# Optimization experiments

Measured on AMD Instinct MI355X. Metric: run time of the kernel, lower is better.

## Reference

```python
import jax, jax.numpy as jnp
import numpy as np

B, T, N, C = 4, 12, 200, 64
ATT = 128      # hard-coded attention_dim in GCN_OPERATION
H = 64         # AdjGen LSTM hidden size
DA = 64        # AdjGen adjacency projection dim
OUT_F = 128    # num_of_out_features
PRED = 12      # predict_length
NFILT = 3      # len(filters) per STSGCM
DATA_LEN = T - 4  # after 2 STSGCL layers


def setup_inputs() -> dict:
    key = jax.random.key(0)
    ks = jax.random.split(key, 16)
    s = 0.05
    f32 = jnp.float32
    return {
        "x": jax.random.normal(ks[0], (B, T, N, C), f32),
        "cur_epi": 5,
        "his_hn": jax.random.normal(ks[1], (B, H), f32),
        "his_cn": jax.random.normal(ks[2], (B, H), f32),
        "Wqkv": jax.random.normal(ks[3], (C, 3 * ATT), f32) * s,
        "bqkv": jnp.zeros((3 * ATT,), f32),
        "Wlin": jax.random.normal(ks[4], (ATT, C), f32) * s,
        "blin": jnp.zeros((C,), f32),
        "Wa": jax.random.normal(ks[5], (C, DA), f32) * s,
        "Wb": jax.random.normal(ks[6], (C, DA), f32) * s,
        "Wx_lstm": jax.random.normal(ks[7], (C, 4 * H), f32) * s,
        "Wh_lstm": jax.random.normal(ks[8], (H, 4 * H), f32) * s,
        "b_lstm": jnp.zeros((4 * H,), f32),
        "temb0": jax.random.normal(ks[9], (1, T, 1, C), f32) * 0.01,
        "temb1": jax.random.normal(ks[10], (1, T - 2, 1, C), f32) * 0.01,
        "semb": jax.random.normal(ks[11], (1, 1, N, C), f32) * 0.01,
        "Wo": jax.random.normal(ks[12], (DATA_LEN * C, OUT_F), f32) * s,
        "bo": jnp.zeros((OUT_F,), f32),
    }


def _forward(x, his_hn, his_cn, Wqkv, bqkv, Wlin, blin, Wa, Wb,
             Wx_lstm, Wh_lstm, b_lstm, temb0, temb1, semb, Wo, bo):
    dt = x.dtype
    att_scale = jnp.sqrt(jnp.asarray(float(ATT), dt))
    adj_scale = jnp.sqrt(jnp.asarray(float(DA), dt))

    def adjgen(xw):
        # xw: (B, nw, M, C). Stand-in for AdjGen (source unavailable):
        # content-dependent learned adjacency over M=3N nodes + one LSTM step.
        node = xw.mean(axis=(0, 1))                                  # (M, C)
        logits = (node @ Wa) @ (node @ Wb).T / adj_scale             # (M, M)
        adj = jax.nn.sigmoid(logits)
        pooled = xw.mean(axis=(1, 2))                                # (B, C)
        gates = pooled @ Wx_lstm + his_hn @ Wh_lstm + b_lstm
        i, f, g, o = jnp.split(gates, 4, axis=-1)
        c_n = jax.nn.sigmoid(f) * his_cn + jax.nn.sigmoid(i) * jnp.tanh(g)
        h_n = jax.nn.sigmoid(o) * jnp.tanh(c_n)
        return adj, logits, h_n, c_n

    def gcn_op(xw, adj):
        # QK^T softmax attention rescaled by adj, renormalized, then AV.
        Bn, nw, M, Cc = xw.shape
        xf = xw.reshape(Bn * nw, M, Cc)
        qkv = xf @ Wqkv + bqkv
        q, k, v = jnp.split(qkv, 3, axis=-1)                          # (BW, M, ATT)
        scores = jnp.einsum('bmd,bnd->bmn', q, k) / att_scale         # (BW, M, M)
        aw = jax.nn.softmax(scores, axis=-1) * adj
        ssum = aw.sum(-1, keepdims=True)
        mask = (ssum > 0).astype(dt)
        w = aw / (ssum + 1e-8) * mask
        out = jnp.einsum('bmn,bnd->bmd', w, jax.nn.relu(v)) @ Wlin + blin
        return out.reshape(Bn, nw, M, -1)

    def stsgcm(xw, Nn):
        cands = []
        cur = xw
        hn = cn = None
        for _ in range(NFILT):
            adj, _logits, hn, cn = adjgen(cur)
            cur = gcn_op(cur, adj)
            Bn, nw, M, F = cur.shape
            # keep only the middle-window copy of the N vertices: [2N:3N]
            cands.append(cur.reshape(Bn * nw, M, F)[:, 2 * Nn:3 * Nn, :])
        out = jnp.max(jnp.stack(cands, axis=0), axis=0)               # (B*nw, N, F)
        return out, hn, cn

    def stsgcl(xw, temb):
        Bn, Tt, Nn, Cc = xw.shape
        xw = xw + temb + semb                                         # position embedding
        nw = Tt - 2
        idx = jnp.arange(nw)[:, None] + jnp.arange(3)[None, :]        # (nw, 3)
        t_all = xw[:, idx].reshape(Bn, nw, 3 * Nn, Cc)
        out, hn, cn = stsgcm(t_all, Nn)
        return out.reshape(Bn, nw, Nn, -1), hn, cn

    h, hn, cn = stsgcl(x, temb0)
    h, hn, cn = stsgcl(h, temb1)
    # OUTPUT layer: (B, T', N, F) -> (B, N, T'*F) -> ReLU(Linear) -> tile PRED times on dim 1
    Bn, Tt, Nn, F = h.shape
    d = h.transpose(0, 2, 1, 3).reshape(Bn, Nn, Tt * F)
    o1 = jax.nn.relu(d @ Wo + bo)                                     # (B, N, OUT_F)
    return jnp.tile(o1, (1, PRED, 1))                                 # (B, PRED*N, OUT_F)


def reference(x, cur_epi, his_hn, his_cn, Wqkv, bqkv, Wlin, blin, Wa, Wb,
              Wx_lstm, Wh_lstm, b_lstm, temb0, temb1, semb, Wo, bo):
    del cur_epi  # annealing schedule of the (unavailable) AdjGen; unused here
    return _forward(x, his_hn, his_cn, Wqkv, bqkv, Wlin, blin, Wa, Wb,
                    Wx_lstm, Wh_lstm, b_lstm, temb0, temb1, semb, Wo, bo)
```

## Files before the change

### kernel.cpp

```cpp
#include <hip/hip_runtime.h>
#include <hip/hip_bf16.h>
#include <math.h>

constexpr int Bc   = 4;
constexpr int Nc   = 200;
constexpr int Cc   = 64;
constexpr int Mc   = 600;
constexpr int ATTc = 128;
constexpr int OUTFc = 128;
constexpr int PREDc = 12;
constexpr int MAXBW = 40;
constexpr int MPAD  = 640;

typedef short short4v __attribute__((ext_vector_type(4)));
typedef short short8 __attribute__((ext_vector_type(8)));
typedef float f32x4  __attribute__((ext_vector_type(4)));

static __device__ __forceinline__ void bsplit(float v, short& h, short& l) {
    __hip_bfloat16 hb = __float2bfloat16(v);
    float hf = __bfloat162float(hb);
    __hip_bfloat16 lb = __float2bfloat16(v - hf);
    h = *(short*)&hb; l = *(short*)&lb;
}

__global__ __launch_bounds__(256)
void embed_window_k(const float* __restrict__ src, const float* __restrict__ temb,
                    const float* __restrict__ semb, float* __restrict__ dst,
                    int Tin, int nw, long total)
{
    long idx = (long)blockIdx.x * 256 + threadIdx.x;
    if (idx >= total) return;
    int c = (int)(idx & 63);
    long r = idx >> 6;
    int n = (int)(r % Nc); r /= Nc;
    int j = (int)(r % 3);  r /= 3;
    int w = (int)(r % nw);
    int b = (int)(r / nw);
    int t = w + j;
    dst[idx] = src[(((long)b * Tin + t) * Nc + n) * Cc + c]
             + temb[t * Cc + c] + semb[n * Cc + c];
}

__global__ __launch_bounds__(256)
void mean_nab_k(const float* __restrict__ cur, const float* __restrict__ Wa,
                const float* __restrict__ Wb,
                ushort* __restrict__ NAH, ushort* __restrict__ NAL,
                ushort* __restrict__ NBH, ushort* __restrict__ NBL, int BW)
{
    __shared__ float Ns[64][17];
    __shared__ float Ws[64][132];
    const int m0 = blockIdx.x * 16;
    const int t = threadIdx.x;
    for (int e = t; e < 1024; e += 256) {
        int r = e >> 4, c4 = (e & 15) << 2;
        *(float4*)&Ws[r][c4]      = *(const float4*)&Wa[r * 64 + c4];
        *(float4*)&Ws[r][64 + c4] = *(const float4*)&Wb[r * 64 + c4];
    }
    {
        int row = t >> 4, c4 = (t & 15) << 2;
        int gm = m0 + row;
        float4 sv = make_float4(0.f, 0.f, 0.f, 0.f);
        if (gm < Mc) {
            for (int bw = 0; bw < BW; bw++) {
                const float4 v = *(const float4*)&cur[((long)bw * Mc + gm) * Cc + c4];
                sv.x += v.x; sv.y += v.y; sv.z += v.z; sv.w += v.w;
            }
        }
        const float inv = 1.f / BW;
        Ns[c4 + 0][row] = sv.x * inv; Ns[c4 + 1][row] = sv.y * inv;
        Ns[c4 + 2][row] = sv.z * inv; Ns[c4 + 3][row] = sv.w * inv;
    }
    __syncthreads();
    const int row = t >> 4, c8 = (t & 15) * 8;
    float acc[8] = {};
    for (int k = 0; k < 64; k++) {
        float a = Ns[k][row];
        float b[8];
        *(float4*)&b[0] = *(const float4*)&Ws[k][c8];
        *(float4*)&b[4] = *(const float4*)&Ws[k][c8 + 4];
#pragma unroll
        for (int j = 0; j < 8; j++) acc[j] += a * b[j];
    }
    int gm = m0 + row;
    if (gm < Mc) {
#pragma unroll
        for (int j = 0; j < 8; j++) {
            int col = c8 + j;
            short h, l;
            bsplit(acc[j], h, l);
            if (col < 64) { NAH[gm * 64 + col] = (ushort)h; NAL[gm * 64 + col] = (ushort)l; }
            else { NBH[gm * 64 + col - 64] = (ushort)h; NBL[gm * 64 + col - 64] = (ushort)l; }
        }
    }
}

__global__ __launch_bounds__(256)
void prep_k(const float* __restrict__ Wlin,
            ushort* __restrict__ WTH, ushort* __restrict__ WTL,
            const float* __restrict__ Wqkv,
            ushort* __restrict__ WQH, ushort* __restrict__ WQL)
{
    int i = blockIdx.x * 256 + threadIdx.x;
    if (i < 64 * 128) {
        int c = i >> 7, a = i & 127;
        short h, l;
        bsplit(Wlin[a * 64 + c], h, l);
        WTH[c * 128 + a] = (ushort)h;
        WTL[c * 128 + a] = (ushort)l;
    } else {
        int j = i - 64 * 128;
        if (j < 384 * 64) {
            int n = j >> 6, c = j & 63;
            short h, l;
            bsplit(Wqkv[c * 384 + n], h, l);
            WQH[n * 64 + c] = (ushort)h;
            WQL[n * 64 + c] = (ushort)l;
        }
    }
}

__global__ __launch_bounds__(256)
void qkv_adj_k(const float* __restrict__ CURp,
               const ushort* __restrict__ WQH, const ushort* __restrict__ WQL,
               const float* __restrict__ bias,
               ushort* __restrict__ QH, ushort* __restrict__ QL,
               ushort* __restrict__ KH, ushort* __restrict__ KL,
               ushort* __restrict__ VTH, ushort* __restrict__ VTL,
               const ushort* __restrict__ Ah, const ushort* __restrict__ Al,
               const ushort* __restrict__ Bh, const ushort* __restrict__ Bl,
               float* __restrict__ ADJ, int nqkv)
{
    __shared__ __align__(16) ushort SM[36864];
    const int t = threadIdx.x;
    const int lane = t & 63, w = t >> 6;
    const int lm = lane & 15, lq = lane >> 4;

    if ((int)blockIdx.x >= nqkv) {
        const int b2 = blockIdx.x - nqkv;
        const int m0 = (b2 / 5) * 128, n0 = (b2 % 5) * 128;
        ushort (*As)[128][40] = (ushort (*)[128][40])(SM);
        ushort (*Bs)[128][40] = (ushort (*)[128][40])(SM + 10240);
        const int wm = (w >> 1) * 64, wn = (w & 1) * 64;

        f32x4 acc[4][4];
#pragma unroll
        for (int i = 0; i < 4; i++)
#pragma unroll
            for (int j = 0; j < 4; j++)
#pragma unroll
                for (int r = 0; r < 4; r++) acc[i][j][r] = 0.f;

        for (int k0 = 0; k0 < 64; k0 += 32) {
            __syncthreads();
#pragma unroll
            for (int p = 0; p < 2; p++) {
                int e = t + p * 256;
                int row = e >> 2, ks = (e & 3) << 3;
                {
                    int gm = m0 + row;
                    short8 vh, vl;
#pragma unroll
                    for (int q = 0; q < 8; q++) { vh[q] = 0; vl[q] = 0; }
                    if (gm < Mc) {
                        vh = *(const short8*)(Ah + (long)gm * 64 + k0 + ks);
                        vl = *(const short8*)(Al + (long)gm * 64 + k0 + ks);
                    }
                    *(short8*)&As[0][row][ks] = vh;
                    *(short8*)&As[1][row][ks] = vl;
                }
                {
                    int gn = n0 + row;
                    short8 vh, vl;
#pragma unroll
                    for (int q = 0; q < 8; q++) { vh[q] = 0; vl[q] = 0; }
                    if (gn < Mc) {
                        vh = *(const short8*)(Bh + (long)gn * 64 + k0 + ks);
                        vl = *(const short8*)(Bl + (long)gn * 64 + k0 + ks);
                    }
                    *(short8*)&Bs[0][row][ks] = vh;
                    *(short8*)&Bs[1][row][ks] = vl;
                }
            }
            __syncthreads();

            short8 af[4][2], bf[4][2];
#pragma unroll
            for (int i = 0; i < 4; i++) {
                af[i][0] = *(const short8*)&As[0][wm + i * 16 + lm][lq * 8];
                af[i][1] = *(const short8*)&As[1][wm + i * 16 + lm][lq * 8];
            }
#pragma unroll
            for (int j = 0; j < 4; j++) {
                bf[j][0] = *(const short8*)&Bs[0][wn + j * 16 + lm][lq * 8];
                bf[j][1] = *(const short8*)&Bs[1][wn + j * 16 + lm][lq * 8];
            }
#pragma unroll
            for (int i = 0; i < 4; i++)
#pragma unroll
                for (int j = 0; j < 4; j++) {
                    acc[i][j] = __builtin_amdgcn_mfma_f32_16x16x32_bf16(af[i][0], bf[j][0], acc[i][j], 0, 0, 0);
                    acc[i][j] = __builtin_amdgcn_mfma_f32_16x16x32_bf16(af[i][0], bf[j][1], acc[i][j], 0, 0, 0);
                    acc[i][j] = __builtin_amdgcn_mfma_f32_16x16x32_bf16(af[i][1], bf[j][0], acc[i][j], 0, 0, 0);
                }
        }
#pragma unroll
        for (int i = 0; i < 4; i++) {
            int gmb = m0 + wm + i * 16 + lq * 4;
#pragma unroll
            for (int j = 0; j < 4; j++) {
                int gn = n0 + wn + j * 16 + lm;
                if (gn >= Mc) continue;
#pragma unroll
                for (int r = 0; r < 4; r++) {
                    int gm = gmb + r;
                    if (gm < Mc)
                        ADJ[(long)gm * Mc + gn] = 1.f / (1.f + __expf(-acc[i][j][r] * 0.125f));
                }
            }
        }
        return;
    }

    ushort* AsH = SM;
    ushort* AsL = SM + 9216;
    ushort* BsH = SM + 18432;
    ushort* BsL = SM + 27648;
    const int bid = blockIdx.x;
    const int xcd = bid & 7, slot = bid >> 3;
    const int z = (slot / 15) * 8 + xcd;
    const int r15 = slot % 15;
    const int which = r15 % 3;
    const int m0 = (r15 / 3) * 128;
    const int nb = which * 128;
    const float* A = CURp + (long)z * Mc * Cc;
    const int wm = (w >> 1) * 64, wn = (w & 1) * 64;

#pragma unroll
    for (int p = 0; p < 8; p++) {
        int e = t + p * 256;
        int row = e >> 4, k4 = (e & 15) * 4;
        int gm = m0 + row;
        float4 v = make_float4(0.f, 0.f, 0.f, 0.f);
        if (gm < Mc) v = *(const float4*)(A + (long)gm * 64 + k4);
        short4v h4, l4;
        short hs, ls;
        bsplit(v.x, hs, ls); h4[0] = hs; l4[0] = ls;
        bsplit(v.y, hs, ls); h4[1] = hs; l4[1] = ls;
        bsplit(v.z, hs, ls); h4[2] = hs; l4[2] = ls;
        bsplit(v.w, hs, ls); h4[3] = hs; l4[3] = ls;
        *(short4v*)(AsH + row * 72 + k4) = h4;
        *(short4v*)(AsL + row * 72 + k4) = l4;
    }
#pragma unroll
    for (int p = 0; p < 4; p++) {
        int e = t + p * 256;
        int row = e >> 3, seg = (e & 7) * 8;
        *(short8*)(BsH + row * 72 + seg) = *(const short8*)(WQH + (long)(nb + row) * 64 + seg);
        *(short8*)(BsL + row * 72 + seg) = *(const short8*)(WQL + (long)(nb + row) * 64 + seg);
    }
    __syncthreads();

    f32x4 acc[4][4];
#pragma unroll
    for (int i = 0; i < 4; i++)
#pragma unroll
        for (int j = 0; j < 4; j++)
#pragma unroll
            for (int r = 0; r < 4; r++) acc[i][j][r] = 0.f;

#pragma unroll
    for (int ks = 0; ks < 2; ks++) {
        short8 af[4][2], bf[4][2];
#pragma unroll
        for (int i = 0; i < 4; i++) {
            af[i][0] = *(const short8*)(AsH + (wm + i * 16 + lm) * 72 + ks * 32 + lq * 8);
            af[i][1] = *(const short8*)(AsL + (wm + i * 16 + lm) * 72 + ks * 32 + lq * 8);
        }
#pragma unroll
        for (int j = 0; j < 4; j++) {
            bf[j][0] = *(const short8*)(BsH + (wn + j * 16 + lm) * 72 + ks * 32 + lq * 8);
            bf[j][1] = *(const short8*)(BsL + (wn + j * 16 + lm) * 72 + ks * 32 + lq * 8);
        }
#pragma unroll
        for (int i = 0; i < 4; i++)
#pragma unroll
            for (int j = 0; j < 4; j++) {
                acc[i][j] = __builtin_amdgcn_mfma_f32_16x16x32_bf16(af[i][0], bf[j][0], acc[i][j], 0, 0, 0);
                acc[i][j] = __builtin_amdgcn_mfma_f32_16x16x32_bf16(af[i][0], bf[j][1], acc[i][j], 0, 0, 0);
                acc[i][j] = __builtin_amdgcn_mfma_f32_16x16x32_bf16(af[i][1], bf[j][0], acc[i][j], 0, 0, 0);
            }
    }
    __syncthreads();

    uint* CP = (uint*)SM;
#pragma unroll
    for (int i = 0; i < 4; i++)
#pragma unroll
        for (int j = 0; j < 4; j++) {
            int col = wn + j * 16 + lm;
            float b = bias[nb + col];
#pragma unroll
            for (int r = 0; r < 4; r++) {
                int row = wm + i * 16 + lq * 4 + r;
                float v = acc[i][j][r] + b;
                if (which == 2) v = fmaxf(v, 0.f);
                short hs, ls;
                bsplit(v, hs, ls);
                CP[row * 132 + col] = ((uint)(ushort)ls << 16) | (uint)(ushort)hs;
            }
        }
    __syncthreads();

    if (which == 2) {
        ushort* vh = VTH + (long)z * ATTc * MPAD;
        ushort* vl = VTL + (long)z * ATTc * MPAD;
#pragma unroll
        for (int p = 0; p < 8; p++) {
            int e = t + p * 256;
            int col = e >> 4, rg = (e & 15) * 8;
            if (m0 + rg < Mc) {
                short8 h8, l8;
#pragma unroll
                for (int q = 0; q < 8; q++) {
                    uint u = CP[(rg + q) * 132 + col];
                    h8[q] = (short)(u & 0xffff);
                    l8[q] = (short)(u >> 16);
                }
                *(short8*)(vh + (long)col * MPAD + m0 + rg) = h8;
                *(short8*)(vl + (long)col * MPAD + m0 + rg) = l8;
            }
        }
    } else {
        ushort* dh = (which == 0 ? QH : KH) + (long)z * Mc * ATTc;
        ushort* dl = (which == 0 ? QL : KL) + (long)z * Mc * ATTc;
#pragma unroll
        for (int p = 0; p < 8; p++) {
            int e = t + p * 256;
            int row = e >> 4, seg = (e & 15) * 8;
            int gm = m0 + row;
            if (gm < Mc) {
                short8 h8, l8;
#pragma unroll
                for (int q = 0; q < 8; q++) {
                    uint u = CP[row * 132 + seg + q];
                    h8[q] = (short)(u & 0xffff);
                    l8[q] = (short)(u >> 16);
                }
                *(short8*)(dh + (long)gm * ATTc + seg) = h8;
                *(short8*)(dl + (long)gm * ATTc + seg) = l8;
            }
        }
    }
}

#define ISSUE_K(Dh, Dl, kc_, g_)                                        \
  _Pragma("unroll")                                                     \
  for (int p = 0; p < 4; p++) {                                         \
    int key = (kc_) + srow0 + 32 * p;                                   \
    short8 vh, vl;                                                      \
    _Pragma("unroll")                                                   \
    for (int q2 = 0; q2 < 8; q2++) { vh[q2] = 0; vl[q2] = 0; }          \
    if (key < Mc) {                                                     \
      vh = *(const short8*)(Khz + (long)key * ATTc + (g_) * 64 + sks);  \
      vl = *(const short8*)(Klz + (long)key * ATTc + (g_) * 64 + sks);  \
    }                                                                   \
    Dh[p] = vh; Dl[p] = vl;                                             \
  }

#define ISSUE_V(Dh, Dl, kc_, g_)                                                   \
  _Pragma("unroll")                                                                \
  for (int p = 0; p < 4; p++) {                                                    \
    int att = srow0 + 32 * p;                                                      \
    Dh[p] = *(const short8*)(Vhz + (long)att * MPAD + (kc_) + (g_) * 64 + sks);    \
    Dl[p] = *(const short8*)(Vlz + (long)att * MPAD + (kc_) + (g_) * 64 + sks);    \
  }

#define WRITE_SB(Dh, Dl)                                                \
  _Pragma("unroll")                                                     \
  for (int p = 0; p < 4; p++) {                                         \
    *(short8*)&SB[0][srow0 + 32 * p][sks] = Dh[p];                      \
    *(short8*)&SB[1][srow0 + 32 * p][sks] = Dl[p];                      \
  }

#define MFMA_QK(base_)                                                   \
  _Pragma("unroll")                                                      \
  for (int kk = 0; kk < 2; kk++) {                                       \
    _Pragma("unroll")                                                    \
    for (int j = 0; j < 8; j++) {                                        \
      short8 bh = *(const short8*)&SB[0][j * 16 + lm][kk * 32 + lq * 8]; \
      short8 bl = *(const short8*)&SB[1][j * 16 + lm][kk * 32 + lq * 8]; \
      sacc[j] = __builtin_amdgcn_mfma_f32_16x16x32_bf16(qh[(base_) + kk], bh, sacc[j], 0, 0, 0); \
      sacc[j] = __builtin_amdgcn_mfma_f32_16x16x32_bf16(qh[(base_) + kk], bl, sacc[j], 0, 0, 0); \
      sacc[j] = __builtin_amdgcn_mfma_f32_16x16x32_bf16(ql[(base_) + kk], bh, sacc[j], 0, 0, 0); \
    }                                                                    \
  }

#define MFMA_PV(g_)                                                      \
  _Pragma("unroll")                                                      \
  for (int kk = 0; kk < 2; kk++) {                                       \
    int po = ((g_) * 64 + kk * 32 + lq * 8) ^ ((lm >> 2) << 3);          \
    short8 ph = *(const short8*)&PH[w][lm][po];                          \
    short8 pl = *(const short8*)&PL[w][lm][po];                          \
    _Pragma("unroll")                                                    \
    for (int j = 0; j < 8; j++) {                                        \
      short8 vh = *(const short8*)&SB[0][j * 16 + lm][kk * 32 + lq * 8]; \
      short8 vl = *(const short8*)&SB[1][j * 16 + lm][kk * 32 + lq * 8]; \
      oacc[j] = __builtin_amdgcn_mfma_f32_16x16x32_bf16(ph, vh, oacc[j], 0, 0, 0); \
      oacc[j] = __builtin_amdgcn_mfma_f32_16x16x32_bf16(ph, vl, oacc[j], 0, 0, 0); \
      oacc[j] = __builtin_amdgcn_mfma_f32_16x16x32_bf16(pl, vh, oacc[j], 0, 0, 0); \
    }                                                                    \
  }

__global__ __launch_bounds__(256, 2)
void attn_k(const ushort* __restrict__ QH, const ushort* __restrict__ QL,
            const ushort* __restrict__ KH, const ushort* __restrict__ KL,
            const ushort* __restrict__ VTH, const ushort* __restrict__ VTL,
            const float* __restrict__ adj, uint* __restrict__ OB, float scale)
{
    __shared__ __align__(16) ushort SB[2][128][72];
    __shared__ __align__(16) ushort PH[4][16][152];
    __shared__ __align__(16) ushort PL[4][16][152];
    const int bid = blockIdx.x;
    const int xcd = bid & 7, slot = bid >> 3;
    const int z = (slot / 10) * 8 + xcd;
    const int m0 = (slot % 10) * 64;
    const int t = threadIdx.x;
    const int lane = t & 63, w = t >> 6;
    const int lm = lane & 15, lq = lane >> 4;
    const int qrow0 = m0 + w * 16;
    const int srow0 = t >> 3;
    const int sks   = (t & 7) << 3;

    const ushort* Qhz = QH + (long)z * Mc * ATTc;
    const ushort* Qlz = QL + (long)z * Mc * ATTc;
    const ushort* Khz = KH + (long)z * Mc * ATTc;
    const ushort* Klz = KL + (long)z * Mc * ATTc;
    const ushort* Vhz = VTH + (long)z * ATTc * MPAD;
    const ushort* Vlz = VTL + (long)z * ATTc * MPAD;

    short8 RAh[4], RAl[4], RBh[4], RBl[4];
    ISSUE_K(RAh, RAl, 0, 0);

    short8 qh[4], ql[4];
    {
        int qr = qrow0 + lm;
        if (qr < Mc) {
            const ushort* qp = Qhz + (long)qr * ATTc;
            const ushort* qp2 = Qlz + (long)qr * ATTc;
#pragma unroll
            for (int ks = 0; ks < 4; ks++) {
                qh[ks] = *(const short8*)(qp + ks * 32 + lq * 8);
                ql[ks] = *(const short8*)(qp2 + ks * 32 + lq * 8);
            }
        } else {
#pragma unroll
            for (int ks = 0; ks < 4; ks++)
#pragma unroll
                for (int q = 0; q < 8; q++) { qh[ks][q] = 0; ql[ks][q] = 0; }
        }
    }

    f32x4 oacc[8];
#pragma unroll
    for (int j = 0; j < 8; j++)
#pragma unroll
        for (int r = 0; r < 4; r++) oacc[j][r] = 0.f;
    float Er[4] = {}, Sr[4] = {};
    float adjv[8][4];

    for (int c = 0; c < 5; c++) {
        const int kc = c * 128;
        f32x4 sacc[8];
#pragma unroll
        for (int j = 0; j < 8; j++)
#pragma unroll
            for (int r = 0; r < 4; r++) sacc[j][r] = 0.f;

        __syncthreads();
        WRITE_SB(RAh, RAl);
        ISSUE_K(RBh, RBl, kc, 1);
#pragma unroll
        for (int j = 0; j < 8; j++) {
            int col = kc + j * 16 + lm;
#pragma unroll
            for (int r = 0; r < 4; r++) {
                int row = qrow0 + lq * 4 + r;
                adjv[j][r] = (col < Mc && row < Mc) ? adj[(long)row * Mc + col] : 0.f;
            }
        }
        __syncthreads();
        MFMA_QK(0);

        __syncthreads();
        WRITE_SB(RBh, RBl);
        ISSUE_V(RAh, RAl, kc, 0);
        __syncthreads();
        MFMA_QK(2);

#pragma unroll
        for (int j = 0; j < 8; j++) {
            int col = kc + j * 16 + lm;
            bool cok = col < Mc;
#pragma unroll
            for (int r = 0; r < 4; r++) {
                float e = cok ? __expf(sacc[j][r] * scale) : 0.f;
                float p = e * adjv[j][r];
                Er[r] += e; Sr[r] += p;
                short hs, ls;
                bsplit(p, hs, ls);
                int cs = (j * 16 + lm) ^ (lq << 3);
                PH[w][lq * 4 + r][cs] = (ushort)hs;
                PL[w][lq * 4 + r][cs] = (ushort)ls;
            }
        }

        __syncthreads();
        WRITE_SB(RAh, RAl);
        ISSUE_V(RBh, RBl, kc, 1);
        __syncthreads();
        MFMA_PV(0);

        __syncthreads();
        WRITE_SB(RBh, RBl);
        if (c < 4) { ISSUE_K(RAh, RAl, kc + 128, 0); }
        __syncthreads();
        MFMA_PV(1);
    }

#pragma unroll
    for (int mk = 1; mk <= 8; mk <<= 1)
#pragma unroll
        for (int r = 0; r < 4; r++) {
            Er[r] += __shfl_xor(Er[r], mk, 64);
            Sr[r] += __shfl_xor(Sr[r], mk, 64);
        }
    float inv[4];
#pragma unroll
    for (int r = 0; r < 4; r++) inv[r] = 1.f / (Sr[r] + 1e-8f * Er[r]);
    uint* Oz = OB + (long)z * Mc * ATTc;
#pragma unroll
    for (int j = 0; j < 8; j++)
#pragma unroll
        for (int r = 0; r < 4; r++) {
            int row = qrow0 + lq * 4 + r;
            if (row < Mc) {
                float v = oacc[j][r] * inv[r];
                short hs, ls;
                bsplit(v, hs, ls);
                Oz[(long)row * ATTc + j * 16 + lm] =
                    ((uint)(ushort)ls << 16) | (uint)(ushort)hs;
            }
        }
}

#undef ISSUE_K
#undef ISSUE_V
#undef WRITE_SB
#undef MFMA_QK
#undef MFMA_PV

__global__ __launch_bounds__(256)
void wlin_k(const uint* __restrict__ OB, const ushort* __restrict__ WTH,
            const ushort* __restrict__ WTL, const float* __restrict__ blin,
            float* __restrict__ CUR, int Mtot,
            float* __restrict__ cand, int first)
{
    __shared__ __align__(16) ushort As[2][128][40];
    __shared__ __align__(16) ushort Bs[2][64][136];
    const int m0 = blockIdx.x * 128;
    const int t = threadIdx.x;
    const int lane = t & 63, w = t >> 6;
    const int wm = (w >> 1) * 64, wn = (w & 1) * 32;
    const int lm = lane & 15, lq = lane >> 4;

#pragma unroll
    for (int p = 0; p < 4; p++) {
        int e = t + p * 256;
        int row = e >> 4, seg = (e & 15) << 3;
        *(short8*)&Bs[0][row][seg] = *(const short8*)(WTH + row * 128 + seg);
        *(short8*)&Bs[1][row][seg] = *(const short8*)(WTL + row * 128 + seg);
    }

    f32x4 acc[4][2];
#pragma unroll
    for (int i = 0; i < 4; i++)
#pragma unroll
        for (int j = 0; j < 2; j++)
#pragma unroll
            for (int r = 0; r < 4; r++) acc[i][j][r] = 0.f;

    for (int k0 = 0; k0 < 128; k0 += 32) {
        __syncthreads();
#pragma unroll
        for (int p = 0; p < 2; p++) {
            int e = t + p * 256;
            int row = e >> 2, seg = (e & 3) << 3;
            int gm = m0 + row;
            short8 vh, vl;
#pragma unroll
            for (int q = 0; q < 8; q++) { vh[q] = 0; vl[q] = 0; }
            if (gm < Mtot) {
                const uint4 u0 = *(const uint4*)(OB + (long)gm * 128 + k0 + seg);
                const uint4 u1 = *(const uint4*)(OB + (long)gm * 128 + k0 + seg + 4);
#pragma unroll
                for (int q = 0; q < 4; q++) {
                    uint u = ((const uint*)&u0)[q];
                    vh[q] = (short)(u & 0xffff); vl[q] = (short)(u >> 16);
                }
#pragma unroll
                for (int q = 0; q < 4; q++) {
                    uint u = ((const uint*)&u1)[q];
                    vh[4 + q] = (short)(u & 0xffff); vl[4 + q] = (short)(u >> 16);
                }
            }
            *(short8*)&As[0][row][seg] = vh;
            *(short8*)&As[1][row][seg] = vl;
        }
        __syncthreads();

        short8 af[4][2], bf[2][2];
#pragma unroll
        for (int i = 0; i < 4; i++) {
            af[i][0] = *(const short8*)&As[0][wm + i * 16 + lm][lq * 8];
            af[i][1] = *(const short8*)&As[1][wm + i * 16 + lm][lq * 8];
        }
#pragma unroll
        for (int j = 0; j < 2; j++) {
            bf[j][0] = *(const short8*)&Bs[0][wn + j * 16 + lm][k0 + lq * 8];
            bf[j][1] = *(const short8*)&Bs[1][wn + j * 16 + lm][k0 + lq * 8];
        }
#pragma unroll
        for (int i = 0; i < 4; i++)
#pragma unroll
            for (int j = 0; j < 2; j++) {
                acc[i][j] = __builtin_amdgcn_mfma_f32_16x16x32_bf16(af[i][0], bf[j][0], acc[i][j], 0, 0, 0);
                acc[i][j] = __builtin_amdgcn_mfma_f32_16x16x32_bf16(af[i][0], bf[j][1], acc[i][j], 0, 0, 0);
                acc[i][j] = __builtin_amdgcn_mfma_f32_16x16x32_bf16(af[i][1], bf[j][0], acc[i][j], 0, 0, 0);
            }
    }
#pragma unroll
    for (int i = 0; i < 4; i++) {
        int gmb = m0 + wm + i * 16 + lq * 4;
#pragma unroll
        for (int j = 0; j < 2; j++) {
            int col = wn + j * 16 + lm;
            float b = blin[col];
#pragma unroll
            for (int r = 0; r < 4; r++) {
                int gm = gmb + r;
                if (gm < Mtot) {
                    float v = acc[i][j][r] + b;
                    CUR[(long)gm * 64 + col] = v;
                    int bw = gm / Mc;
                    int m = gm - bw * Mc;
                    if (m >= 2 * Nc) {
                        long o = ((long)bw * Nc + (m - 2 * Nc)) * Cc + col;
                        cand[o] = first ? v : fmaxf(cand[o], v);
                    }
                }
            }
        }
    }
}

__global__ __launch_bounds__(128)
void output_k(const float* __restrict__ h2, const float* __restrict__ Wo,
              const float* __restrict__ bo, float* __restrict__ out)
{
    __shared__ float ds[512];
    int row = blockIdx.x;
    int b = row / Nc, n = row % Nc;
    int t = threadIdx.x;
    for (int e = t; e < 512; e += 128) {
        int tt = e >> 6, c = e & 63;
        ds[e] = h2[(((long)b * 8 + tt) * Nc + n) * Cc + c];
    }
    __syncthreads();
    float acc = bo[t];
    for (int e = 0; e < 512; e++) acc += ds[e] * Wo[e * OUTFc + t];
    acc = fmaxf(acc, 0.f);
    for (int p = 0; p < PREDc; p++)
        out[(((long)b * PREDc + p) * Nc + n) * (long)OUTFc + t] = acc;
}

extern "C" void kernel_launch(void* const* d_in, const int* in_sizes, int n_in,
                              void* d_out, int out_size, void* d_ws, size_t ws_size,
                              hipStream_t stream)
{
    (void)in_sizes; (void)n_in; (void)out_size; (void)ws_size;
    const float* x     = (const float*)d_in[0];
    const float* Wqkv  = (const float*)d_in[4];
    const float* bqkv  = (const float*)d_in[5];
    const float* Wlin  = (const float*)d_in[6];
    const float* blin  = (const float*)d_in[7];
    const float* Wa    = (const float*)d_in[8];
    const float* Wb    = (const float*)d_in[9];
    const float* temb0 = (const float*)d_in[13];
    const float* temb1 = (const float*)d_in[14];
    const float* semb  = (const float*)d_in[15];
    const float* Wo    = (const float*)d_in[16];
    const float* bo    = (const float*)d_in[17];
    float* out = (float*)d_out;

    float* ws   = (float*)d_ws;
    float* CUR  = ws;
    float* ADJ  = CUR + (long)MAXBW * Mc * Cc;
    float* CAND = ADJ + (long)Mc * Mc;
    uint*  OB   = (uint*)(CAND + (long)MAXBW * Nc * Cc);
    float* QHf  = (float*)(OB + (long)MAXBW * Mc * ATTc);
    const long QSZ = (long)MAXBW * Mc * ATTc / 2;
    float* QLf  = QHf + QSZ;
    float* KHf  = QLf + QSZ;
    float* KLf  = KHf + QSZ;
    float* VTHf = KLf + QSZ;
    float* VTLf = VTHf + (long)MAXBW * ATTc * MPAD / 2;
    ushort* NAH = (ushort*)(VTLf + (long)MAXBW * ATTc * MPAD / 2);
    ushort* NAL = NAH + Mc * Cc;
    ushort* NBH = NAL + Mc * Cc;
    ushort* NBL = NBH + Mc * Cc;
    ushort* WTH = NBL + Mc * Cc;
    ushort* WTL = WTH + 64 * 128;
    ushort* WQH = WTL + 64 * 128;
    ushort* WQL = WQH + 384 * 64;

    ushort* QH  = (ushort*)QHf;
    ushort* QL  = (ushort*)QLf;
    ushort* KH  = (ushort*)KHf;
    ushort* KL  = (ushort*)KLf;
    ushort* VTH = (ushort*)VTHf;
    ushort* VTL = (ushort*)VTLf;

    const float inv_sqrt_att = 0.08838834764831845f;

    prep_k<<<dim3(128), dim3(256), 0, stream>>>(Wlin, WTH, WTL, Wqkv, WQH, WQL);

    for (int layer = 0; layer < 2; layer++) {
        int Tin = layer ? 10 : 12;
        int nw  = Tin - 2;
        int BW  = Bc * nw;
        int Mtot = BW * Mc;
        const float* src  = layer ? CAND : x;
        const float* temb = layer ? temb1 : temb0;

        long etotal = (long)BW * Mc * Cc;
        embed_window_k<<<dim3((unsigned)((etotal + 255) / 256)), dim3(256), 0, stream>>>(
            src, temb, semb, CUR, Tin, nw, etotal);

        for (int it = 0; it < 3; it++) {
            mean_nab_k<<<dim3(38), dim3(256), 0, stream>>>(
                CUR, Wa, Wb, NAH, NAL, NBH, NBL, BW);

            int nqkv = BW * 15;
            qkv_adj_k<<<dim3(nqkv + 25), dim3(256), 0, stream>>>(
                CUR, WQH, WQL, bqkv, QH, QL, KH, KL, VTH, VTL,
                NAH, NAL, NBH, NBL, ADJ, nqkv);

            attn_k<<<dim3(BW * 10), dim3(256), 0, stream>>>(
                QH, QL, KH, KL, VTH, VTL, ADJ, OB, inv_sqrt_att);

            wlin_k<<<dim3((Mtot + 127) / 128), dim3(256), 0, stream>>>(
                OB, WTH, WTL, blin, CUR, Mtot, CAND, it == 0 ? 1 : 0);
        }
    }
    output_k<<<dim3(Bc * Nc), dim3(128), 0, stream>>>(CAND, Wo, bo, out);
}
```

Baseline: 722.0 us.

## Fuse output linear projection into attention kernel epilogue

```diff
diff --git a/kernel.cpp b/kernel.cpp
--- a/kernel.cpp
+++ b/kernel.cpp
@@ -415,11 +415,18 @@
 void attn_k(const ushort* __restrict__ QH, const ushort* __restrict__ QL,
             const ushort* __restrict__ KH, const ushort* __restrict__ KL,
             const ushort* __restrict__ VTH, const ushort* __restrict__ VTL,
-            const float* __restrict__ adj, uint* __restrict__ OB, float scale)
+            const float* __restrict__ adj,
+            const ushort* __restrict__ WTH, const ushort* __restrict__ WTL,
+            const float* __restrict__ blin,
+            float* __restrict__ CUR, float* __restrict__ cand, int first,
+            float scale)
 {
-    __shared__ __align__(16) ushort SB[2][128][72];
-    __shared__ __align__(16) ushort PH[4][16][152];
-    __shared__ __align__(16) ushort PL[4][16][152];
+    __shared__ __align__(16) ushort SMEM[37888];
+    typedef ushort sb_t[128][72];
+    typedef ushort ph_t[16][152];
+    sb_t* SB = (sb_t*)SMEM;
+    ph_t* PH = (ph_t*)(SMEM + 18432);
+    ph_t* PL = (ph_t*)(SMEM + 28160);
     const int bid = blockIdx.x;
     const int xcd = bid & 7, slot = bid >> 3;
     const int z = (slot / 10) * 8 + xcd;
@@ -537,20 +544,82 @@
     float inv[4];
 #pragma unroll
     for (int r = 0; r < 4; r++) inv[r] = 1.f / (Sr[r] + 1e-8f * Er[r]);
-    uint* Oz = OB + (long)z * Mc * ATTc;
+
+    __syncthreads();
+    uint*   OP  = (uint*)SMEM;
+    ushort* BsF = SMEM + 16896;
+
+#pragma unroll
+    for (int p = 0; p < 4; p++) {
+        int e = t + p * 256;
+        int row = e >> 4, seg = (e & 15) << 3;
+        *(short8*)(BsF + row * 136 + seg) = *(const short8*)(WTH + row * 128 + seg);
+        *(short8*)(BsF + 64 * 136 + row * 136 + seg) = *(const short8*)(WTL + row * 128 + seg);
+    }
 #pragma unroll
     for (int j = 0; j < 8; j++)
 #pragma unroll
         for (int r = 0; r < 4; r++) {
-            int row = qrow0 + lq * 4 + r;
+            int lrow = w * 16 + lq * 4 + r;
+            float v = oacc[j][r] * inv[r];
+            short hs, ls;
+            bsplit(v, hs, ls);
+            OP[lrow * 132 + j * 16 + lm] = ((uint)(ushort)ls << 16) | (uint)(ushort)hs;
+        }
+    __syncthreads();
+
+    f32x4 cacc[4];
+#pragma unroll
+    for (int jj = 0; jj < 4; jj++)
+#pragma unroll
+        for (int r = 0; r < 4; r++) cacc[jj][r] = 0.f;
+
+#pragma unroll
+    for (int ks = 0; ks < 4; ks++) {
+        short8 ah, al;
+        {
+            const uint* src = OP + (w * 16 + lm) * 132 + ks * 32 + lq * 8;
+            const uint4 u0 = *(const uint4*)src;
+            const uint4 u1 = *(const uint4*)(src + 4);
+#pragma unroll
+            for (int q = 0; q < 4; q++) {
+                uint u = ((const uint*)&u0)[q];
+                ah[q] = (short)(u & 0xffff); al[q] = (short)(u >> 16);
+            }
+#pragma unroll
+            for (int q = 0; q < 4; q++) {
+                uint u = ((const uint*)&u1)[q];
+                ah[4 + q] = (short)(u & 0xffff); al[4 + q] = (short)(u >> 16);
+            }
+        }
+#pragma unroll
+        for (int jj = 0; jj < 4; jj++) {
+            short8 bh = *(const short8*)(BsF + (jj * 16 + lm) * 136 + ks * 32 + lq * 8);
+            short8 bl = *(const short8*)(BsF + 64 * 136 + (jj * 16 + lm) * 136 + ks * 32 + lq * 8);
+            cacc[jj] = __builtin_amdgcn_mfma_f32_16x16x32_bf16(ah, bh, cacc[jj], 0, 0, 0);
+            cacc[jj] = __builtin_amdgcn_mfma_f32_16x16x32_bf16(ah, bl, cacc[jj], 0, 0, 0);
+            cacc[jj] = __builtin_amdgcn_mfma_f32_16x16x32_bf16(al, bh, cacc[jj], 0, 0, 0);
+        }
+    }
+
+    float* CURz = CUR + (long)z * Mc * Cc;
+#pragma unroll
+    for (int jj = 0; jj < 4; jj++) {
+        int col = jj * 16 + lm;
+        float b = blin[col];
+#pragma unroll
+        for (int r = 0; r < 4; r++) {
+            int row = m0 + w * 16 + lq * 4 + r;
             if (row < Mc) {
-                float v = oacc[j][r] * inv[r];
-                short hs, ls;
-                bsplit(v, hs, ls);
-                Oz[(long)row * ATTc + j * 16 + lm] =
-                    ((uint)(ushort)ls << 16) | (uint)(ushort)hs;
-            }
-        }
+                float v = cacc[jj][r] + b;
+                CURz[(long)row * Cc + col] = v;
+                if (row >= 2 * Nc) {
+                    long o = ((long)z * Nc + (row - 2 * Nc)) * Cc + col;
+                    cand[o] = first ? v : fmaxf(cand[o], v);
+                }
+            }
+        }
+    }
 }
 
 #undef ISSUE_K
@@ -558,110 +627,6 @@
 #undef WRITE_SB
 #undef MFMA_QK
 #undef MFMA_PV
-
-__global__ __launch_bounds__(256)
-void wlin_k(const uint* __restrict__ OB, const ushort* __restrict__ WTH,
-            const ushort* __restrict__ WTL, const float* __restrict__ blin,
-            float* __restrict__ CUR, int Mtot,
-            float* __restrict__ cand, int first)
-{
-    __shared__ __align__(16) ushort As[2][128][40];
-    __shared__ __align__(16) ushort Bs[2][64][136];
-    const int m0 = blockIdx.x * 128;
-    const int t = threadIdx.x;
-    const int lane = t & 63, w = t >> 6;
-    const int wm = (w >> 1) * 64, wn = (w & 1) * 32;
-    const int lm = lane & 15, lq = lane >> 4;
-
-#pragma unroll
-    for (int p = 0; p < 4; p++) {
-        int e = t + p * 256;
-        int row = e >> 4, seg = (e & 15) << 3;
-        *(short8*)&Bs[0][row][seg] = *(const short8*)(WTH + row * 128 + seg);
-        *(short8*)&Bs[1][row][seg] = *(const short8*)(WTL + row * 128 + seg);
-    }
-
-    f32x4 acc[4][2];
-#pragma unroll
-    for (int i = 0; i < 4; i++)
-#pragma unroll
-        for (int j = 0; j < 2; j++)
-#pragma unroll
-            for (int r = 0; r < 4; r++) acc[i][j][r] = 0.f;
-
-    for (int k0 = 0; k0 < 128; k0 += 32) {
-        __syncthreads();
-#pragma unroll
-        for (int p = 0; p < 2; p++) {
-            int e = t + p * 256;
-            int row = e >> 2, seg = (e & 3) << 3;
-            int gm = m0 + row;
-            short8 vh, vl;
-#pragma unroll
-            for (int q = 0; q < 8; q++) { vh[q] = 0; vl[q] = 0; }
-            if (gm < Mtot) {
-                const uint4 u0 = *(const uint4*)(OB + (long)gm * 128 + k0 + seg);
-                const uint4 u1 = *(const uint4*)(OB + (long)gm * 128 + k0 + seg + 4);
-#pragma unroll
-                for (int q = 0; q < 4; q++) {
-                    uint u = ((const uint*)&u0)[q];
-                    vh[q] = (short)(u & 0xffff); vl[q] = (short)(u >> 16);
-                }
-#pragma unroll
-                for (int q = 0; q < 4; q++) {
-                    uint u = ((const uint*)&u1)[q];
-                    vh[4 + q] = (short)(u & 0xffff); vl[4 + q] = (short)(u >> 16);
-                }
-            }
-            *(short8*)&As[0][row][seg] = vh;
-            *(short8*)&As[1][row][seg] = vl;
-        }
-        __syncthreads();
-
-        short8 af[4][2], bf[2][2];
-#pragma unroll
-        for (int i = 0; i < 4; i++) {
-            af[i][0] = *(const short8*)&As[0][wm + i * 16 + lm][lq * 8];
-            af[i][1] = *(const short8*)&As[1][wm + i * 16 + lm][lq * 8];
-        }
-#pragma unroll
-        for (int j = 0; j < 2; j++) {
-            bf[j][0] = *(const short8*)&Bs[0][wn + j * 16 + lm][k0 + lq * 8];
-            bf[j][1] = *(const short8*)&Bs[1][wn + j * 16 + lm][k0 + lq * 8];
-        }
-#pragma unroll
-        for (int i = 0; i < 4; i++)
-#pragma unroll
-            for (int j = 0; j < 2; j++) {
-                acc[i][j] = __builtin_amdgcn_mfma_f32_16x16x32_bf16(af[i][0], bf[j][0], acc[i][j], 0, 0, 0);
-                acc[i][j] = __builtin_amdgcn_mfma_f32_16x16x32_bf16(af[i][0], bf[j][1], acc[i][j], 0, 0, 0);
-                acc[i][j] = __builtin_amdgcn_mfma_f32_16x16x32_bf16(af[i][1], bf[j][0], acc[i][j], 0, 0, 0);
-            }
-    }
-#pragma unroll
-    for (int i = 0; i < 4; i++) {
-        int gmb = m0 + wm + i * 16 + lq * 4;
-#pragma unroll
-        for (int j = 0; j < 2; j++) {
-            int col = wn + j * 16 + lm;
-            float b = blin[col];
-#pragma unroll
-            for (int r = 0; r < 4; r++) {
-                int gm = gmb + r;
-                if (gm < Mtot) {
-                    float v = acc[i][j][r] + b;
-                    CUR[(long)gm * 64 + col] = v;
-                    int bw = gm / Mc;
-                    int m = gm - bw * Mc;
-                    if (m >= 2 * Nc) {
-                        long o = ((long)bw * Nc + (m - 2 * Nc)) * Cc + col;
-                        cand[o] = first ? v : fmaxf(cand[o], v);
-                    }
-                }
-            }
-        }
-    }
-}
 
 __global__ __launch_bounds__(128)
 void output_k(const float* __restrict__ h2, const float* __restrict__ Wo,
@@ -738,7 +703,6 @@
         int Tin = layer ? 10 : 12;
         int nw  = Tin - 2;
         int BW  = Bc * nw;
-        int Mtot = BW * Mc;
         const float* src  = layer ? CAND : x;
         const float* temb = layer ? temb1 : temb0;
 
@@ -756,10 +720,8 @@
                 NAH, NAL, NBH, NBL, ADJ, nqkv);
 
             attn_k<<<dim3(BW * 10), dim3(256), 0, stream>>>(
-                QH, QL, KH, KL, VTH, VTL, ADJ, OB, inv_sqrt_att);
-
-            wlin_k<<<dim3((Mtot + 127) / 128), dim3(256), 0, stream>>>(
-                OB, WTH, WTL, blin, CUR, Mtot, CAND, it == 0 ? 1 : 0);
+                QH, QL, KH, KL, VTH, VTL, ADJ, WTH, WTL, blin,
+                CUR, CAND, it == 0 ? 1 : 0, inv_sqrt_att);
         }
     }
     output_k<<<dim3(Bc * Nc), dim3(128), 0, stream>>>(CAND, Wo, bo, out);
```

Result: faster. 647.4 us (-10.3%).
